# Optimization experiments

Hardware: AMD Instinct MI355X
Metric: run time of the kernel (lower is better)

The kernel has to match this reference:

```python
import jax, jax.numpy as jnp
import numpy as np

KERNEL = 3
PAD = KERNEL // 2  # 1


def cal_wfft_ortho(weight, n, cout, cin):
    # weight: [N, M, k, k] with M < N
    nf = n // 2 + 1
    vfft = jnp.fft.rfft2(weight, s=(n, n), norm='ortho')          # [N, M, n, nf] complex
    vfft = jnp.transpose(vfft, (2, 3, 0, 1))                       # [n, nf, N, M]
    vH = jnp.conj(jnp.swapaxes(vfft, -1, -2))                      # [n, nf, M, N]
    wfft = vH @ vfft                                               # [n, nf, M, M] Gram
    perturb_ratio = 1e-5
    eps = jnp.mean(jnp.diagonal(wfft, axis1=-2, axis2=-1), axis=-1) * perturb_ratio
    m = wfft.shape[-1]
    wfft = wfft + eps[..., None, None] * jnp.eye(m, dtype=wfft.dtype)
    N = vfft.shape[-2]
    I = jnp.eye(N, dtype=wfft.dtype)
    # Cayley-style orthogonal projector: I - 2 V (V^H V)^{-1} V^H
    ortho = I - 2.0 * (vfft @ jnp.linalg.solve(wfft, vH))          # [n, nf, N, N]
    ortho = ortho[:, :, :cout, :cin]
    return ortho.reshape(n * nf, cout, cin)


def setup_inputs() -> dict:
    key = jax.random.key(0)
    k1, k2, k3 = jax.random.split(key, 3)
    B, C, H = 64, 256, 32
    x = jax.random.normal(k1, (B, C, H, H), dtype=jnp.float32)
    # masked low-rank orthogonal weight: [cout, cin-1, 3, 3]
    weight = jax.random.normal(k2, (C, C - 1, KERNEL, KERNEL), dtype=jnp.float32) * 0.05
    bias = jax.random.normal(k3, (C,), dtype=jnp.float32) * 0.01
    return {"x": x, "weight": weight, "bias": bias}


def reference(x, weight, bias):
    B, cin, h, _ = x.shape
    cout = weight.shape[0]
    xp = jnp.pad(x, ((0, 0), (0, 0), (PAD, PAD), (PAD, PAD)))
    n = h + 2 * PAD
    nf = n // 2 + 1
    # x to frequency domain: [n*nf, cin, B]
    xfft = jnp.fft.rfft2(xp, norm='ortho')                         # [B, cin, n, nf]
    xfft = jnp.transpose(xfft, (2, 3, 1, 0)).reshape(n * nf, cin, B)
    W = cal_wfft_ortho(weight, n, cout, cin)                       # [n*nf, cout, cin]
    zfft = W @ xfft                                                # [n*nf, cout, B]
    zfft = jnp.transpose(zfft.reshape(n, nf, cout, B), (3, 2, 0, 1))
    z = jnp.fft.irfft2(zfft, norm='ortho')                         # [B, cout, n, n] real
    z = z[:, :, PAD:-PAD, PAD:-PAD]
    z = z + bias[:, None, None]
    return z
```

## Files before the change

### kernel.cpp

```cpp
#include <hip/hip_runtime.h>
#include <math.h>

#define NN    34
#define NFH   18
#define NFREQ 612
#define CH    256
#define CIN   255
#define NB    64
#define HW    32
#define PI2   6.2831853071795864769f
#define TSTRIDE 36864

__device__ __forceinline__ int tIdx(int I, int J){ return ((I*(I+1))>>1) + J; }

__global__ __launch_bounds__(256) void kF1(const float* __restrict__ x, float2* __restrict__ U){
  __shared__ float tc[NFH][HW], ts[NFH][HW];
  int tid = threadIdx.x;
  for (int i = tid; i < NFH*HW; i += 256){
    int kx = i >> 5, w = i & 31;
    float s, c; sincosf(-PI2*(float)(kx*(w+1))/34.f, &s, &c);
    tc[kx][w] = c; ts[kx][w] = s;
  }
  __syncthreads();
  int c = blockIdx.x;
  int a = (blockIdx.y << 2) + (tid >> 6);
  int b = tid & 63;
  const float4* xr = (const float4*)(x + (((size_t)b*CH + c)*HW + a)*HW);
  float xv[HW];
#pragma unroll
  for (int t = 0; t < 8; t++){
    float4 v = xr[t];
    xv[4*t] = v.x; xv[4*t+1] = v.y; xv[4*t+2] = v.z; xv[4*t+3] = v.w;
  }
#pragma unroll 1
  for (int kx = 0; kx < NFH; kx++){
    float re = 0.f, im = 0.f;
#pragma unroll
    for (int w = 0; w < HW; w++){ re += xv[w]*tc[kx][w]; im += xv[w]*ts[kx][w]; }
    U[(((size_t)a*NFH + kx)*CH + c)*NB + b] = make_float2(re, im);
  }
}

__global__ __launch_bounds__(512) void kF2(const float2* __restrict__ U, float2* __restrict__ X){
  __shared__ float pc[NN][HW], ps[NN][HW];
  int tid = threadIdx.x;
  for (int i = tid; i < NN*HW; i += 512){
    int ky = i >> 5, a = i & 31;
    float s, c; sincosf(-PI2*(float)(ky*(a+1))/34.f, &s, &c);
    pc[ky][a] = c*(1.f/34.f); ps[ky][a] = s*(1.f/34.f);
  }
  __syncthreads();
  int kx = blockIdx.x;
  int c  = (blockIdx.y << 3) + (tid >> 6);
  int b  = tid & 63;
  float2 u[HW];
#pragma unroll
  for (int a = 0; a < HW; a++) u[a] = U[(((size_t)a*NFH + kx)*CH + c)*NB + b];
#pragma unroll 1
  for (int ky = 0; ky < NN; ky++){
    float re = 0.f, im = 0.f;
#pragma unroll
    for (int a = 0; a < HW; a++){
      float cc = pc[ky][a], ss = ps[ky][a];
      re += u[a].x*cc - u[a].y*ss;
      im += u[a].x*ss + u[a].y*cc;
    }
    X[(((size_t)ky*NFH + kx)*CH + c)*NB + b] = make_float2(re, im);
  }
}

__global__ __launch_bounds__(256) void kT0(const float* __restrict__ w, float* __restrict__ wT){
  int idx = blockIdx.x*256 + threadIdx.x;
  if (idx >= 9*CH*CIN) return;
  int k = idx / (CH*CIN);
  int r = idx - k*(CH*CIN);
  wT[idx] = w[(size_t)r*9 + k];
}

__global__ __launch_bounds__(256) void kC(const float* __restrict__ wT, float* __restrict__ C2){
  int kk = blockIdx.x;
  int k1 = kk / 9, k2 = kk - k1*9;
  int to = (blockIdx.y >> 2) << 6, tp = (blockIdx.y & 3) << 6;
  __shared__ float As[64][33], Bs[64][33];
  int tid = threadIdx.x;
  int ty = tid >> 4, tx = tid & 15;
  float acc[4][4] = {};
  const float* Ab = wT + (size_t)k1*CH*CIN;
  const float* Bb = wT + (size_t)k2*CH*CIN;
  for (int i0 = 0; i0 < CIN; i0 += 32){
    for (int idx = tid; idx < 64*32; idx += 256){
      int r = idx >> 5, j = idx & 31;
      int i = i0 + j;
      As[r][j] = (i < CIN) ? Ab[(size_t)(to + r)*CIN + i] : 0.f;
      Bs[r][j] = (i < CIN) ? Bb[(size_t)(tp + r)*CIN + i] : 0.f;
    }
    __syncthreads();
#pragma unroll
    for (int j = 0; j < 32; j++){
      float av[4], bv[4];
#pragma unroll
      for (int d = 0; d < 4; d++){ av[d] = As[ty*4+d][j]; bv[d] = Bs[tx*4+d][j]; }
#pragma unroll
      for (int da = 0; da < 4; da++)
#pragma unroll
        for (int db = 0; db < 4; db++) acc[da][db] += av[da]*bv[db];
    }
    __syncthreads();
  }
  float* Cb = C2 + (size_t)kk*CH*CH;
#pragma unroll
  for (int da = 0; da < 4; da++)
#pragma unroll
    for (int db = 0; db < 4; db++)
      Cb[(size_t)(to + ty*4 + da)*CH + tp + tx*4 + db] = acc[da][db];
}

__global__ __launch_bounds__(64) void kM(const float* __restrict__ C2, float2* __restrict__ M, int cf0, int cF){
  int t = blockIdx.x;
  int I = 0;
  while ((((I+1)*(I+2))>>1) <= t) I++;
  int J = t - ((I*(I+1))>>1);
  int r = blockIdx.y;
  int o = I*32 + r, p0 = J*32;
  int fl = (blockIdx.z << 6) + threadIdx.x;
  bool act = fl < cF;
  int f = act ? (cf0 + fl) : 0;
  int ky = f / NFH, kx = f - ky*NFH;
  float Pc[5], Ps[5], Qc[5], Qs[5];
#pragma unroll
  for (int d = 0; d < 5; d++){
    float s, c;
    sincosf(-PI2*(float)(ky*(d-2))/34.f, &s, &c);
    Pc[d] = c*(1.f/1156.f); Ps[d] = s*(1.f/1156.f);
    sincosf(-PI2*(float)(kx*(d-2))/34.f, &s, &c);
    Qc[d] = c; Qs[d] = s;
  }
  float ax[32] = {}, ay[32] = {};
  const float* Cb = C2 + (size_t)o*CH + p0;
#pragma unroll 1
  for (int k1 = 0; k1 < 9; k1++){
#pragma unroll 1
    for (int k2 = 0; k2 < 9; k2++){
      int da = k1/3 - k2/3 + 2, db = k1%3 - k2%3 + 2;
      float cr = Pc[da]*Qc[db] - Ps[da]*Qs[db];
      float ci = Pc[da]*Qs[db] + Ps[da]*Qc[db];
      const float* crow = Cb + (size_t)(k1*9 + k2)*CH*CH;
#pragma unroll
      for (int j = 0; j < 32; j++){
        float cv = crow[j];
        ax[j] += cv*cr; ay[j] += cv*ci;
      }
    }
  }
  if (act){
    float2* Mr = M + (size_t)fl*TSTRIDE + ((size_t)t << 10) + (r << 5);
#pragma unroll
    for (int j = 0; j < 32; j++) Mr[j] = make_float2(ax[j], ay[j]);
  }
}

__global__ __launch_bounds__(256) void kEps(float2* __restrict__ M, float* __restrict__ eb, int cf0){
  int fi = blockIdx.x;
  int o = threadIdx.x;
  int I = o >> 5, r = o & 31;
  float2* Mf = M + (size_t)fi*TSTRIDE + ((size_t)tIdx(I,I) << 10) + r*32 + r;
  __shared__ float red[256];
  float d = Mf->x;
  red[o] = d;
  __syncthreads();
  for (int s = 128; s > 0; s >>= 1){ if (o < s) red[o] += red[o+s]; __syncthreads(); }
  float eps = red[0] * (1e-5f/255.f);
  Mf->x = d + eps;
  if (o == 0) eb[cf0 + fi] = eps;
}

__global__ __launch_bounds__(256) void kStep(float2* __restrict__ Mg, int k, int cF){
  __shared__ float2 As[32][33], Bs[32][33];
  __shared__ float2 colbuf[2][32];
  __shared__ float darr[32];
  int fi = blockIdx.x;
  float2* Tf = Mg + (size_t)fi*TSTRIDE;
  int tid = threadIdx.x;
  if (blockIdx.y == 0){
    const int h = CH - (k << 5);
    const bool act = tid < h;
    float2* rowp = Tf + ((size_t)tIdx(k + (tid >> 5), k) << 10) + ((tid & 31) << 5);
    float2 r[32];
    if (act){
#pragma unroll
      for (int t = 0; t < 16; t++){
        float4 v = ((const float4*)rowp)[t];
        r[2*t]   = make_float2(v.x, v.y);
        r[2*t+1] = make_float2(v.z, v.w);
      }
    }
    if (k > 0){
      const float2* ts2 = Tf + ((size_t)tIdx(k, k-1) << 10);
      for (int idx = tid; idx < 1024; idx += 256)
        As[idx >> 5][idx & 31] = ts2[idx];
      __syncthreads();
      if (act){
        const float4* lqp = (const float4*)(Tf + ((size_t)tIdx(k + (tid >> 5), k-1) << 10) + ((tid & 31) << 5));
#pragma unroll 1
        for (int c4 = 0; c4 < 4; c4++){
          float2 lq[8];
#pragma unroll
          for (int t = 0; t < 4; t++){
            float4 v = lqp[c4*4 + t];
            lq[2*t]   = make_float2(v.x, v.y);
            lq[2*t+1] = make_float2(v.z, v.w);
          }
#pragma unroll 4
          for (int j = 0; j < 32; j++){
#pragma unroll
            for (int m = 0; m < 8; m++){
              float2 L = As[j][c4*8 + m];
              r[j].x -= lq[m].x*L.x + lq[m].y*L.y;
              r[j].y -= lq[m].y*L.x - lq[m].x*L.y;
            }
          }
        }
      }
      __syncthreads();
    }
#pragma unroll
    for (int kk = 0; kk < 32; kk++){
      if (act && tid >= kk && tid < 32) colbuf[kk & 1][tid] = r[kk];
      __syncthreads();
      float pinv = __builtin_amdgcn_rcpf(colbuf[kk & 1][kk].x);
      if (act && tid > kk){
        float ax = r[kk].x * pinv, ay = r[kk].y * pinv;
#pragma unroll
        for (int j = kk + 1; j < 32; j++){
          float2 l = colbuf[kk & 1][j];
          r[j].x -= ax*l.x + ay*l.y;
          r[j].y -= ay*l.x - ax*l.y;
        }
      }
    }
    if (act && tid < 32) darr[tid] = r[tid].x;
    __syncthreads();
    if (act){
#pragma unroll
      for (int j = 0; j < 32; j++){
        float sc = __frsqrt_rn(fmaxf(darr[j], 1e-30f));
        r[j].x *= sc; r[j].y *= sc;
      }
#pragma unroll
      for (int t = 0; t < 16; t++)
        ((float4*)rowp)[t] = make_float4(r[2*t].x, r[2*t].y, r[2*t+1].x, r[2*t+1].y);
    }
  } else {
    int p = blockIdx.y - 1;
    int li = 0;
    while ((((li+1)*(li+2)) >> 1) <= p) li++;
    int lj = p - ((li*(li+1)) >> 1);
    int I = k + 1 + li, J = k + 1 + lj;
    const float2* Asrc = Tf + ((size_t)tIdx(I, k-1) << 10);
    const float2* Bsrc = Tf + ((size_t)tIdx(J, k-1) << 10);
    float2* Cdst = Tf + ((size_t)tIdx(I, J) << 10);
    for (int idx = tid; idx < 1024; idx += 256){
      int r2 = idx >> 5, c2 = idx & 31;
      As[r2][c2] = Asrc[idx];
      Bs[r2][c2] = Bsrc[idx];
    }
    int r2 = tid >> 3, c0 = (tid & 7) << 2;
    float2 acc[4];
    float4 c01 = *(const float4*)(Cdst + r2*32 + c0);
    float4 c23 = *(const float4*)(Cdst + r2*32 + c0 + 2);
    acc[0] = make_float2(c01.x, c01.y); acc[1] = make_float2(c01.z, c01.w);
    acc[2] = make_float2(c23.x, c23.y); acc[3] = make_float2(c23.z, c23.w);
    __syncthreads();
#pragma unroll 4
    for (int kk = 0; kk < 32; kk++){
      float2 a = As[r2][kk];
#pragma unroll
      for (int d = 0; d < 4; d++){
        float2 b = Bs[c0 + d][kk];
        acc[d].x -= a.x*b.x + a.y*b.y;
        acc[d].y -= a.y*b.x - a.x*b.y;
      }
    }
    *(float4*)(Cdst + r2*32 + c0)     = make_float4(acc[0].x, acc[0].y, acc[1].x, acc[1].y);
    *(float4*)(Cdst + r2*32 + c0 + 2) = make_float4(acc[2].x, acc[2].y, acc[3].x, acc[3].y);
  }
}


#define VST 12

template<int RB>
__device__ __forceinline__ void updF(float2 (&s)[8][4], const float2* __restrict__ tb,
                                     const float2* __restrict__ vb, int r, int hf){
#pragma unroll 2
  for (int k = 0; k < 32; k++){
    float2 l = tb[r*33 + k];
    const float4* vp = (const float4*)(vb + k*VST + (hf<<2));
    float4 va = vp[0], vb4 = vp[1];
    s[RB][0].x -= l.x*va.x - l.y*va.y;  s[RB][0].y -= l.x*va.y + l.y*va.x;
    s[RB][1].x -= l.x*va.z - l.y*va.w;  s[RB][1].y -= l.x*va.w + l.y*va.z;
    s[RB][2].x -= l.x*vb4.x - l.y*vb4.y; s[RB][2].y -= l.x*vb4.y + l.y*vb4.x;
    s[RB][3].x -= l.x*vb4.z - l.y*vb4.w; s[RB][3].y -= l.x*vb4.w + l.y*vb4.z;
  }
}

template<int RB>
__device__ __forceinline__ void updB(float2 (&s)[8][4], const float2* __restrict__ tb,
                                     const float2* __restrict__ vb, int r, int hf){
#pragma unroll 2
  for (int k = 0; k < 32; k++){
    float2 l = tb[k*33 + r];
    const float4* vp = (const float4*)(vb + k*VST + (hf<<2));
    float4 va = vp[0], vb4 = vp[1];
    s[RB][0].x -= l.x*va.x + l.y*va.y;  s[RB][0].y -= l.x*va.y - l.y*va.x;
    s[RB][1].x -= l.x*va.z + l.y*va.w;  s[RB][1].y -= l.x*va.w - l.y*va.z;
    s[RB][2].x -= l.x*vb4.x + l.y*vb4.y; s[RB][2].y -= l.x*vb4.y - l.y*vb4.x;
    s[RB][3].x -= l.x*vb4.z + l.y*vb4.w; s[RB][3].y -= l.x*vb4.w - l.y*vb4.z;
  }
}

template<int JB>
__device__ __forceinline__ void diagF(float2 (&s)[8][4], const float2* __restrict__ tb,
                                      float2* __restrict__ vb, int r, int hf){
  float2 sv0 = s[JB][0], sv1 = s[JB][1], sv2 = s[JB][2], sv3 = s[JB][3];
  int src = hf << 5;
#pragma unroll 1
  for (int k = 0; k < 32; k++){
    float dinv = __builtin_amdgcn_rcpf(tb[k*33 + k].x);
    float c0x = sv0.x*dinv, c0y = sv0.y*dinv;
    float c1x = sv1.x*dinv, c1y = sv1.y*dinv;
    float c2x = sv2.x*dinv, c2y = sv2.y*dinv;
    float c3x = sv3.x*dinv, c3y = sv3.y*dinv;
    float2 v0, v1, v2, v3;
    v0.x = __shfl(c0x, src + k, 64); v0.y = __shfl(c0y, src + k, 64);
    v1.x = __shfl(c1x, src + k, 64); v1.y = __shfl(c1y, src + k, 64);
    v2.x = __shfl(c2x, src + k, 64); v2.y = __shfl(c2y, src + k, 64);
    v3.x = __shfl(c3x, src + k, 64); v3.y = __shfl(c3y, src + k, 64);
    if (r == k){ sv0 = v0; sv1 = v1; sv2 = v2; sv3 = v3; }
    else if (r > k){
      float2 l = tb[r*33 + k];
      sv0.x -= l.x*v0.x - l.y*v0.y; sv0.y -= l.x*v0.y + l.y*v0.x;
      sv1.x -= l.x*v1.x - l.y*v1.y; sv1.y -= l.x*v1.y + l.y*v1.x;
      sv2.x -= l.x*v2.x - l.y*v2.y; sv2.y -= l.x*v2.y + l.y*v2.x;
      sv3.x -= l.x*v3.x - l.y*v3.y; sv3.y -= l.x*v3.y + l.y*v3.x;
    }
  }
  s[JB][0] = sv0; s[JB][1] = sv1; s[JB][2] = sv2; s[JB][3] = sv3;
  float4* wp = (float4*)(vb + r*VST + (hf<<2));
  wp[0] = make_float4(sv0.x, sv0.y, sv1.x, sv1.y);
  wp[1] = make_float4(sv2.x, sv2.y, sv3.x, sv3.y);
}

template<int JB>
__device__ __forceinline__ void diagB(float2 (&s)[8][4], const float2* __restrict__ tb,
                                      float2* __restrict__ vb, int r, int hf){
  float2 sv0 = s[JB][0], sv1 = s[JB][1], sv2 = s[JB][2], sv3 = s[JB][3];
  int src = hf << 5;
#pragma unroll 1
  for (int k = 31; k >= 0; k--){
    float dinv = __builtin_amdgcn_rcpf(tb[k*33 + k].x);
    float c0x = sv0.x*dinv, c0y = sv0.y*dinv;
    float c1x = sv1.x*dinv, c1y = sv1.y*dinv;
    float c2x = sv2.x*dinv, c2y = sv2.y*dinv;
    float c3x = sv3.x*dinv, c3y = sv3.y*dinv;
    float2 v0, v1, v2, v3;
    v0.x = __shfl(c0x, src + k, 64); v0.y = __shfl(c0y, src + k, 64);
    v1.x = __shfl(c1x, src + k, 64); v1.y = __shfl(c1y, src + k, 64);
    v2.x = __shfl(c2x, src + k, 64); v2.y = __shfl(c2y, src + k, 64);
    v3.x = __shfl(c3x, src + k, 64); v3.y = __shfl(c3y, src + k, 64);
    if (r == k){ sv0 = v0; sv1 = v1; sv2 = v2; sv3 = v3; }
    else if (r < k){
      float2 l = tb[k*33 + r];
      sv0.x -= l.x*v0.x + l.y*v0.y; sv0.y -= l.x*v0.y - l.y*v0.x;
      sv1.x -= l.x*v1.x + l.y*v1.y; sv1.y -= l.x*v1.y - l.y*v1.x;
      sv2.x -= l.x*v2.x + l.y*v2.y; sv2.y -= l.x*v2.y - l.y*v2.x;
      sv3.x -= l.x*v3.x + l.y*v3.y; sv3.y -= l.x*v3.y - l.y*v3.x;
    }
  }
  s[JB][0] = sv0; s[JB][1] = sv1; s[JB][2] = sv2; s[JB][3] = sv3;
  float4* wp = (float4*)(vb + r*VST + (hf<<2));
  wp[0] = make_float4(sv0.x, sv0.y, sv1.x, sv1.y);
  wp[1] = make_float4(sv2.x, sv2.y, sv3.x, sv3.y);
}

#define DISPATCH8(FN, V) \
  switch (V){ \
    case 0: FN<0>(s, tb, vb, r, hf); break; \
    case 1: FN<1>(s, tb, vb, r, hf); break; \
    case 2: FN<2>(s, tb, vb, r, hf); break; \
    case 3: FN<3>(s, tb, vb, r, hf); break; \
    case 4: FN<4>(s, tb, vb, r, hf); break; \
    case 5: FN<5>(s, tb, vb, r, hf); break; \
    case 6: FN<6>(s, tb, vb, r, hf); break; \
    default: FN<7>(s, tb, vb, r, hf); break; }

__global__ __launch_bounds__(128) void kSolve(const float2* __restrict__ Lg, float2* __restrict__ X,
                                              const float* __restrict__ eb, int cf0, int cF){
  __shared__ float2 tb2[2][32*33];
  __shared__ __align__(16) float2 vbuf[2][32*VST];
  __shared__ int seq[72];
  int fi = blockIdx.x;
  if (fi >= cF) return;
  int f = cf0 + fi;
  const float2* Tf = Lg + (size_t)fi*TSTRIDE;
  float2* Xf = X + (size_t)f*CH*NB;
  int tid = threadIdx.x, wv = tid >> 6, lane = tid & 63, hf = lane >> 5, r = lane & 31;
  int cc = (blockIdx.y << 4) + (wv << 3) + (hf << 2);
  if (tid == 0){
    int n = 0;
    for (int jb = 0; jb < 8; jb++){
      seq[n++] = jb | (jb << 4) | (1 << 12);
      for (int ib = jb+1; ib < 8; ib++) seq[n++] = ib | (jb << 4) | (0 << 12);
    }
    for (int jb = 7; jb >= 0; jb--){
      seq[n++] = jb | (jb << 4) | (2 << 12);
      for (int ii = jb-1; ii >= 0; ii--) seq[n++] = jb | (ii << 4) | (3 << 12);
    }
  }
  float2 s[8][4];
#pragma unroll
  for (int rb = 0; rb < 8; rb++){
    const float2* xp = Xf + (size_t)((rb << 5) + r)*NB + cc;
    float4 a = *(const float4*)xp, b = *(const float4*)(xp + 2);
    s[rb][0] = make_float2(a.x, a.y); s[rb][1] = make_float2(a.z, a.w);
    s[rb][2] = make_float2(b.x, b.y); s[rb][3] = make_float2(b.z, b.w);
  }
  {
    const float4* src = (const float4*)(Tf + (tid << 3));
    float4 a0 = src[0], a1 = src[1], a2 = src[2], a3 = src[3];
    int row = tid >> 2, col = (tid & 3) << 3;
    float2* d = &tb2[0][row*33 + col];
    d[0] = make_float2(a0.x, a0.y); d[1] = make_float2(a0.z, a0.w);
    d[2] = make_float2(a1.x, a1.y); d[3] = make_float2(a1.z, a1.w);
    d[4] = make_float2(a2.x, a2.y); d[5] = make_float2(a2.z, a2.w);
    d[6] = make_float2(a3.x, a3.y); d[7] = make_float2(a3.z, a3.w);
  }
  __syncthreads();
  float2* vb = vbuf[wv];
  int cur = 0;
#pragma unroll 1
  for (int t = 0; t < 72; t++){
    float4 p0, p1, p2, p3;
    bool pf = t < 71;
    if (pf){
      int e2 = seq[t+1];
      const float4* src = (const float4*)(Tf + ((size_t)tIdx(e2 & 15, (e2 >> 4) & 15) << 10) + (tid << 3));
      p0 = src[0]; p1 = src[1]; p2 = src[2]; p3 = src[3];
    }
    int e = seq[t];
    int type = e >> 12;
    const float2* tb = tb2[cur];
    if (type == 0){        int rbT = e & 15;        DISPATCH8(updF, rbT); }
    else if (type == 1){   int jb  = e & 15;        DISPATCH8(diagF, jb); }
    else if (type == 2){   int jb  = e & 15;        DISPATCH8(diagB, jb); }
    else {                 int rbT = (e >> 4) & 15; DISPATCH8(updB, rbT); }
    if (pf){
      int row = tid >> 2, col = (tid & 3) << 3;
      float2* d = &tb2[cur ^ 1][row*33 + col];
      d[0] = make_float2(p0.x, p0.y); d[1] = make_float2(p0.z, p0.w);
      d[2] = make_float2(p1.x, p1.y); d[3] = make_float2(p1.z, p1.w);
      d[4] = make_float2(p2.x, p2.y); d[5] = make_float2(p2.z, p2.w);
      d[6] = make_float2(p3.x, p3.y); d[7] = make_float2(p3.z, p3.w);
    }
    __syncthreads();
    cur ^= 1;
  }
  float te = 2.f * eb[f];
#pragma unroll
  for (int rb = 0; rb < 8; rb++){
    float2* xp = Xf + (size_t)((rb << 5) + r)*NB + cc;
    float4 a = *(const float4*)xp, b = *(const float4*)(xp + 2);
    *(float4*)xp       = make_float4(te*s[rb][0].x - a.x, te*s[rb][0].y - a.y,
                                     te*s[rb][1].x - a.z, te*s[rb][1].y - a.w);
    *(float4*)(xp + 2) = make_float4(te*s[rb][2].x - b.x, te*s[rb][2].y - b.y,
                                     te*s[rb][3].x - b.z, te*s[rb][3].y - b.w);
  }
}

__global__ __launch_bounds__(512) void kI1(const float2* __restrict__ X, float2* __restrict__ Y){
  __shared__ float pc[HW][NN], ps[HW][NN];
  int tid = threadIdx.x;
  for (int i = tid; i < HW*NN; i += 512){
    int a = i / NN, ky = i - a*NN;
    float s, c; sincosf(PI2*(float)(ky*(a+1))/34.f, &s, &c);
    pc[a][ky] = c; ps[a][ky] = s;
  }
  __syncthreads();
  int kx = blockIdx.x;
  int cc = (blockIdx.y << 3) + (tid >> 6);
  int b = tid & 63;
  float2 z[NN];
#pragma unroll
  for (int ky = 0; ky < NN; ky++) z[ky] = X[(((size_t)ky*NFH + kx)*CH + cc)*NB + b];
#pragma unroll 1
  for (int a = 0; a < HW; a++){
    float re = 0.f, im = 0.f;
#pragma unroll
    for (int ky = 0; ky < NN; ky++){
      float co = pc[a][ky], si = ps[a][ky];
      re += z[ky].x*co - z[ky].y*si;
      im += z[ky].x*si + z[ky].y*co;
    }
    Y[(((size_t)a*NFH + kx)*CH + cc)*NB + b] = make_float2(re, im);
  }
}

__global__ __launch_bounds__(256) void kI2(const float2* __restrict__ Y, const float* __restrict__ bias,
                                           float* __restrict__ out){
  __shared__ float tc[NFH][HW], tsn[NFH][HW];
  int tid = threadIdx.x;
  for (int i = tid; i < NFH*HW; i += 256){
    int kx = i >> 5, w = i & 31;
    float wt = (kx == 0 || kx == 17) ? (1.f/34.f) : (2.f/34.f);
    float s, c; sincosf(PI2*(float)(kx*(w+1))/34.f, &s, &c);
    tc[kx][w] = wt*c; tsn[kx][w] = wt*s;
  }
  __syncthreads();
  int cc = blockIdx.x;
  int a = (blockIdx.y << 2) + (tid >> 6);
  int b = tid & 63;
  float2 yv[NFH];
#pragma unroll
  for (int kx = 0; kx < NFH; kx++) yv[kx] = Y[(((size_t)a*NFH + kx)*CH + cc)*NB + b];
  float bi = bias[cc];
  float ov[HW];
#pragma unroll
  for (int w = 0; w < HW; w++){
    float acc = bi;
#pragma unroll
    for (int kx = 0; kx < NFH; kx++)
      acc += yv[kx].x*tc[kx][w] - yv[kx].y*tsn[kx][w];
    ov[w] = acc;
  }
  float4* op = (float4*)(out + (((size_t)b*CH + cc)*HW + a)*HW);
#pragma unroll
  for (int t = 0; t < 8; t++) op[t] = make_float4(ov[4*t], ov[4*t+1], ov[4*t+2], ov[4*t+3]);
}

extern "C" void kernel_launch(void* const* d_in, const int* in_sizes, int n_in,
                              void* d_out, int out_size, void* d_ws, size_t ws_size,
                              hipStream_t stream){
  (void)in_sizes; (void)n_in; (void)out_size;
  const float* x    = (const float*)d_in[0];
  const float* w    = (const float*)d_in[1];
  const float* bias = (const float*)d_in[2];
  float* out = (float*)d_out;
  char* ws = (char*)d_ws;

  const size_t X_BYTES  = (size_t)NFREQ*CH*NB*sizeof(float2);
  const size_t WT_BYTES = (size_t)9*CH*CIN*sizeof(float);
  const size_t C_BYTES  = (size_t)81*CH*CH*sizeof(float);
  const size_t offX  = 0;
  const size_t offWT = offX + X_BYTES;
  const size_t offC  = offWT + WT_BYTES;
  const size_t offE  = offC + C_BYTES;
  const size_t offChunk = offE + 4096;
  const size_t perF = (size_t)TSTRIDE * sizeof(float2);

  float2* X  = (float2*)(ws + offX);
  float*  wT = (float*)(ws + offWT);
  float*  C2 = (float*)(ws + offC);
  float*  eb = (float*)(ws + offE);
  float2* U  = (float2*)(ws + offChunk);
  float2* Mb = (float2*)(ws + offChunk);
  float2* Y  = (float2*)(ws + offChunk);

  size_t avail = ws_size > offChunk ? ws_size - offChunk : 0;
  int F = (int)(avail / perF);
  if (F < 1) F = 1;
  if (F > NFREQ) F = NFREQ;
  int nch = (NFREQ + F - 1) / F;
  F = (NFREQ + nch - 1) / nch;

  kF1<<<dim3(CH, 8), 256, 0, stream>>>(x, U);
  kF2<<<dim3(NFH, 32), 512, 0, stream>>>(U, X);
  kT0<<<(9*CH*CIN + 255)/256, 256, 0, stream>>>(w, wT);
  kC<<<dim3(81, 16), 256, 0, stream>>>(wT, C2);

  for (int cf0 = 0; cf0 < NFREQ; cf0 += F){
    int cF = (NFREQ - cf0 < F) ? (NFREQ - cf0) : F;
    kM<<<dim3(36, 32, (cF + 63) >> 6), 64, 0, stream>>>(C2, Mb, cf0, cF);
    kEps<<<cF, 256, 0, stream>>>(Mb, eb, cf0);
    for (int k = 0; k < 8; k++){
      int m = 7 - k;
      int npairs = (k >= 1) ? (m*(m+1)) >> 1 : 0;
      kStep<<<dim3(cF, 1 + npairs), 256, 0, stream>>>(Mb, k, cF);
    }
    int cF8 = (cF + 7) & ~7;
    kSolve<<<dim3(cF8, 4), 128, 0, stream>>>(Mb, X, eb, cf0, cF);
  }

  kI1<<<dim3(NFH, 32), 512, 0, stream>>>(X, Y);
  kI2<<<dim3(CH, 8), 256, 0, stream>>>(Y, bias, out);
}
```

Measured before the change: 3.586 ms.

## Give each wave a private triangular tile buffer and drop block barriers

```diff
diff --git a/kernel.cpp b/kernel.cpp
--- a/kernel.cpp
+++ b/kernel.cpp
@@ -396,7 +396,7 @@
 
 __global__ __launch_bounds__(128) void kSolve(const float2* __restrict__ Lg, float2* __restrict__ X,
                                               const float* __restrict__ eb, int cf0, int cF){
-  __shared__ float2 tb2[2][32*33];
+  __shared__ float2 tbw[2][32*33];
   __shared__ __align__(16) float2 vbuf[2][32*VST];
   __shared__ int seq[72];
   int fi = blockIdx.x;
@@ -425,45 +425,45 @@
     s[rb][0] = make_float2(a.x, a.y); s[rb][1] = make_float2(a.z, a.w);
     s[rb][2] = make_float2(b.x, b.y); s[rb][3] = make_float2(b.z, b.w);
   }
+  float2* tb = tbw[wv];
+  float2* vb = vbuf[wv];
   {
-    const float4* src = (const float4*)(Tf + (tid << 3));
-    float4 a0 = src[0], a1 = src[1], a2 = src[2], a3 = src[3];
-    int row = tid >> 2, col = (tid & 3) << 3;
-    float2* d = &tb2[0][row*33 + col];
-    d[0] = make_float2(a0.x, a0.y); d[1] = make_float2(a0.z, a0.w);
-    d[2] = make_float2(a1.x, a1.y); d[3] = make_float2(a1.z, a1.w);
-    d[4] = make_float2(a2.x, a2.y); d[5] = make_float2(a2.z, a2.w);
-    d[6] = make_float2(a3.x, a3.y); d[7] = make_float2(a3.z, a3.w);
+    const float4* src = (const float4*)Tf;
+#pragma unroll
+    for (int i = 0; i < 8; i++){
+      float4 v = src[i*64 + lane];
+      int g = i*64 + lane;
+      int row = g >> 4, col = (g & 15) << 1;
+      tb[row*33 + col]     = make_float2(v.x, v.y);
+      tb[row*33 + col + 1] = make_float2(v.z, v.w);
+    }
   }
   __syncthreads();
-  float2* vb = vbuf[wv];
-  int cur = 0;
 #pragma unroll 1
   for (int t = 0; t < 72; t++){
-    float4 p0, p1, p2, p3;
+    float4 pf4[8];
     bool pf = t < 71;
     if (pf){
       int e2 = seq[t+1];
-      const float4* src = (const float4*)(Tf + ((size_t)tIdx(e2 & 15, (e2 >> 4) & 15) << 10) + (tid << 3));
-      p0 = src[0]; p1 = src[1]; p2 = src[2]; p3 = src[3];
+      const float4* src = (const float4*)(Tf + ((size_t)tIdx(e2 & 15, (e2 >> 4) & 15) << 10));
+#pragma unroll
+      for (int i = 0; i < 8; i++) pf4[i] = src[i*64 + lane];
     }
     int e = seq[t];
     int type = e >> 12;
-    const float2* tb = tb2[cur];
     if (type == 0){        int rbT = e & 15;        DISPATCH8(updF, rbT); }
     else if (type == 1){   int jb  = e & 15;        DISPATCH8(diagF, jb); }
     else if (type == 2){   int jb  = e & 15;        DISPATCH8(diagB, jb); }
     else {                 int rbT = (e >> 4) & 15; DISPATCH8(updB, rbT); }
     if (pf){
-      int row = tid >> 2, col = (tid & 3) << 3;
-      float2* d = &tb2[cur ^ 1][row*33 + col];
-      d[0] = make_float2(p0.x, p0.y); d[1] = make_float2(p0.z, p0.w);
-      d[2] = make_float2(p1.x, p1.y); d[3] = make_float2(p1.z, p1.w);
-      d[4] = make_float2(p2.x, p2.y); d[5] = make_float2(p2.z, p2.w);
-      d[6] = make_float2(p3.x, p3.y); d[7] = make_float2(p3.z, p3.w);
-    }
-    __syncthreads();
-    cur ^= 1;
+#pragma unroll
+      for (int i = 0; i < 8; i++){
+        int g = i*64 + lane;
+        int row = g >> 4, col = (g & 15) << 1;
+        tb[row*33 + col]     = make_float2(pf4[i].x, pf4[i].y);
+        tb[row*33 + col + 1] = make_float2(pf4[i].z, pf4[i].w);
+      }
+    }
   }
   float te = 2.f * eb[f];
 #pragma unroll
```

Result: no change. 3.609 ms (+0.6%).

## Precompute inverses of diagonal Cholesky blocks to replace serial triangular solves

Applied to the files above, without the earlier changes.

```diff
diff --git a/kernel.cpp b/kernel.cpp
--- a/kernel.cpp
+++ b/kernel.cpp
@@ -286,6 +286,42 @@
   }
 }
 
+__global__ __launch_bounds__(64) void kInv(float2* __restrict__ Mg){
+  __shared__ float2 Ls[32][33];
+  __shared__ float2 Yc[32][33];
+  int fi = blockIdx.x, jb = blockIdx.y;
+  float2* Tfd = Mg + (size_t)fi*TSTRIDE + ((size_t)tIdx(jb, jb) << 10);
+  int lane = threadIdx.x;
+  for (int i = lane; i < 1024; i += 64)
+    Ls[i >> 5][i & 31] = Tfd[i];
+  __syncthreads();
+  if (lane < 32){
+    const int c = lane;
+#pragma unroll 1
+    for (int rr = 0; rr < 32; rr++){
+      float2 v;
+      if (rr < c) v = make_float2(0.f, 0.f);
+      else if (rr == c) v = make_float2(__builtin_amdgcn_rcpf(Ls[c][c].x), 0.f);
+      else {
+        float ax = 0.f, ay = 0.f;
+#pragma unroll 1
+        for (int k = c; k < rr; k++){
+          float2 l = Ls[rr][k];
+          float2 yk = Yc[k][c];
+          ax += l.x*yk.x - l.y*yk.y;
+          ay += l.x*yk.y + l.y*yk.x;
+        }
+        float dinv = __builtin_amdgcn_rcpf(Ls[rr][rr].x);
+        v = make_float2(-ax*dinv, -ay*dinv);
+      }
+      Yc[rr][c] = v;
+    }
+  }
+  __syncthreads();
+  for (int i = lane; i < 1024; i += 64)
+    Tfd[i] = Yc[i >> 5][i & 31];
+}
+
 
 #define VST 12
 
@@ -322,65 +358,49 @@
 template<int JB>
 __device__ __forceinline__ void diagF(float2 (&s)[8][4], const float2* __restrict__ tb,
                                       float2* __restrict__ vb, int r, int hf){
-  float2 sv0 = s[JB][0], sv1 = s[JB][1], sv2 = s[JB][2], sv3 = s[JB][3];
-  int src = hf << 5;
-#pragma unroll 1
+  float4* wp = (float4*)(vb + r*VST + (hf<<2));
+  wp[0] = make_float4(s[JB][0].x, s[JB][0].y, s[JB][1].x, s[JB][1].y);
+  wp[1] = make_float4(s[JB][2].x, s[JB][2].y, s[JB][3].x, s[JB][3].y);
+  __syncthreads();
+  float2 a0 = make_float2(0.f,0.f), a1 = a0, a2 = a0, a3 = a0;
+#pragma unroll 2
   for (int k = 0; k < 32; k++){
-    float dinv = __builtin_amdgcn_rcpf(tb[k*33 + k].x);
-    float c0x = sv0.x*dinv, c0y = sv0.y*dinv;
-    float c1x = sv1.x*dinv, c1y = sv1.y*dinv;
-    float c2x = sv2.x*dinv, c2y = sv2.y*dinv;
-    float c3x = sv3.x*dinv, c3y = sv3.y*dinv;
-    float2 v0, v1, v2, v3;
-    v0.x = __shfl(c0x, src + k, 64); v0.y = __shfl(c0y, src + k, 64);
-    v1.x = __shfl(c1x, src + k, 64); v1.y = __shfl(c1y, src + k, 64);
-    v2.x = __shfl(c2x, src + k, 64); v2.y = __shfl(c2y, src + k, 64);
-    v3.x = __shfl(c3x, src + k, 64); v3.y = __shfl(c3y, src + k, 64);
-    if (r == k){ sv0 = v0; sv1 = v1; sv2 = v2; sv3 = v3; }
-    else if (r > k){
-      float2 l = tb[r*33 + k];
-      sv0.x -= l.x*v0.x - l.y*v0.y; sv0.y -= l.x*v0.y + l.y*v0.x;
-      sv1.x -= l.x*v1.x - l.y*v1.y; sv1.y -= l.x*v1.y + l.y*v1.x;
-      sv2.x -= l.x*v2.x - l.y*v2.y; sv2.y -= l.x*v2.y + l.y*v2.x;
-      sv3.x -= l.x*v3.x - l.y*v3.y; sv3.y -= l.x*v3.y + l.y*v3.x;
-    }
-  }
-  s[JB][0] = sv0; s[JB][1] = sv1; s[JB][2] = sv2; s[JB][3] = sv3;
-  float4* wp = (float4*)(vb + r*VST + (hf<<2));
-  wp[0] = make_float4(sv0.x, sv0.y, sv1.x, sv1.y);
-  wp[1] = make_float4(sv2.x, sv2.y, sv3.x, sv3.y);
+    float2 l = tb[r*33 + k];
+    const float4* vp = (const float4*)(vb + k*VST + (hf<<2));
+    float4 va = vp[0], vb4 = vp[1];
+    a0.x += l.x*va.x - l.y*va.y;  a0.y += l.x*va.y + l.y*va.x;
+    a1.x += l.x*va.z - l.y*va.w;  a1.y += l.x*va.w + l.y*va.z;
+    a2.x += l.x*vb4.x - l.y*vb4.y; a2.y += l.x*vb4.y + l.y*vb4.x;
+    a3.x += l.x*vb4.z - l.y*vb4.w; a3.y += l.x*vb4.w + l.y*vb4.z;
+  }
+  s[JB][0] = a0; s[JB][1] = a1; s[JB][2] = a2; s[JB][3] = a3;
+  __syncthreads();
+  wp[0] = make_float4(a0.x, a0.y, a1.x, a1.y);
+  wp[1] = make_float4(a2.x, a2.y, a3.x, a3.y);
 }
 
 template<int JB>
 __device__ __forceinline__ void diagB(float2 (&s)[8][4], const float2* __restrict__ tb,
                                       float2* __restrict__ vb, int r, int hf){
-  float2 sv0 = s[JB][0], sv1 = s[JB][1], sv2 = s[JB][2], sv3 = s[JB][3];
-  int src = hf << 5;
-#pragma unroll 1
-  for (int k = 31; k >= 0; k--){
-    float dinv = __builtin_amdgcn_rcpf(tb[k*33 + k].x);
-    float c0x = sv0.x*dinv, c0y = sv0.y*dinv;
-    float c1x = sv1.x*dinv, c1y = sv1.y*dinv;
-    float c2x = sv2.x*dinv, c2y = sv2.y*dinv;
-    float c3x = sv3.x*dinv, c3y = sv3.y*dinv;
-    float2 v0, v1, v2, v3;
-    v0.x = __shfl(c0x, src + k, 64); v0.y = __shfl(c0y, src + k, 64);
-    v1.x = __shfl(c1x, src + k, 64); v1.y = __shfl(c1y, src + k, 64);
-    v2.x = __shfl(c2x, src + k, 64); v2.y = __shfl(c2y, src + k, 64);
-    v3.x = __shfl(c3x, src + k, 64); v3.y = __shfl(c3y, src + k, 64);
-    if (r == k){ sv0 = v0; sv1 = v1; sv2 = v2; sv3 = v3; }
-    else if (r < k){
-      float2 l = tb[k*33 + r];
-      sv0.x -= l.x*v0.x + l.y*v0.y; sv0.y -= l.x*v0.y - l.y*v0.x;
-      sv1.x -= l.x*v1.x + l.y*v1.y; sv1.y -= l.x*v1.y - l.y*v1.x;
-      sv2.x -= l.x*v2.x + l.y*v2.y; sv2.y -= l.x*v2.y - l.y*v2.x;
-      sv3.x -= l.x*v3.x + l.y*v3.y; sv3.y -= l.x*v3.y - l.y*v3.x;
-    }
-  }
-  s[JB][0] = sv0; s[JB][1] = sv1; s[JB][2] = sv2; s[JB][3] = sv3;
   float4* wp = (float4*)(vb + r*VST + (hf<<2));
-  wp[0] = make_float4(sv0.x, sv0.y, sv1.x, sv1.y);
-  wp[1] = make_float4(sv2.x, sv2.y, sv3.x, sv3.y);
+  wp[0] = make_float4(s[JB][0].x, s[JB][0].y, s[JB][1].x, s[JB][1].y);
+  wp[1] = make_float4(s[JB][2].x, s[JB][2].y, s[JB][3].x, s[JB][3].y);
+  __syncthreads();
+  float2 a0 = make_float2(0.f,0.f), a1 = a0, a2 = a0, a3 = a0;
+#pragma unroll 2
+  for (int k = 0; k < 32; k++){
+    float2 l = tb[k*33 + r];
+    const float4* vp = (const float4*)(vb + k*VST + (hf<<2));
+    float4 va = vp[0], vb4 = vp[1];
+    a0.x += l.x*va.x + l.y*va.y;  a0.y += l.x*va.y - l.y*va.x;
+    a1.x += l.x*va.z + l.y*va.w;  a1.y += l.x*va.w - l.y*va.z;
+    a2.x += l.x*vb4.x + l.y*vb4.y; a2.y += l.x*vb4.y - l.y*vb4.x;
+    a3.x += l.x*vb4.z + l.y*vb4.w; a3.y += l.x*vb4.w - l.y*vb4.z;
+  }
+  s[JB][0] = a0; s[JB][1] = a1; s[JB][2] = a2; s[JB][3] = a3;
+  __syncthreads();
+  wp[0] = make_float4(a0.x, a0.y, a1.x, a1.y);
+  wp[1] = make_float4(a2.x, a2.y, a3.x, a3.y);
 }
 
 #define DISPATCH8(FN, V) \
@@ -586,6 +606,7 @@
       int npairs = (k >= 1) ? (m*(m+1)) >> 1 : 0;
       kStep<<<dim3(cF, 1 + npairs), 256, 0, stream>>>(Mb, k, cF);
     }
+    kInv<<<dim3(cF, 8), 64, 0, stream>>>(Mb);
     int cF8 = (cF + 7) & ~7;
     kSolve<<<dim3(cF8, 4), 128, 0, stream>>>(Mb, X, eb, cf0, cF);
   }
```

Result: faster. 3.440 ms (-4.1%).
